# Kernel tuning notes

Measured on AMD Instinct MI355X. Metric: run time of the kernel, lower is better.

The kernel has to match this reference:

```python
import jax, jax.numpy as jnp
import numpy as np
import math

B, S, E, A = 8, 2048, 1024, 1024
NEG = -1e20

def setup_inputs() -> dict:
    key = jax.random.key(0)
    ks = jax.random.split(key, 6)
    scale = 1.0 / math.sqrt(E)
    return {
        "q": jax.random.normal(ks[0], (B, S, E), dtype=jnp.float32),
        "k": jax.random.normal(ks[1], (B, S, E), dtype=jnp.float32),
        "v": jax.random.normal(ks[2], (B, S, E), dtype=jnp.float32),
        "mask_pad": jnp.ones((B, S, S), dtype=jnp.int32),
        "Wq": jax.random.normal(ks[3], (E, A), dtype=jnp.float32) * scale,
        "Wk": jax.random.normal(ks[4], (E, A), dtype=jnp.float32) * scale,
        "Wv": jax.random.normal(ks[5], (E, A), dtype=jnp.float32) * scale,
    }

def reference(q, k, v, mask_pad, Wq, Wk, Wv):
    att_dim = Wq.shape[1]
    qp = jnp.einsum('bse,ea->bsa', q, Wq)
    kp = jnp.einsum('bse,ea->bsa', k, Wk)
    vp = jnp.einsum('bse,ea->bsa', v, Wv)
    # scores: [B, S, S]
    qk = jnp.einsum('bqa,bka->bqk', qp, kp) / jnp.sqrt(jnp.float32(att_dim))
    qk = jnp.where(mask_pad == 0, NEG, qk)
    # causal: torch.tril zeros out upper triangle, then zeros -> -1e20 (faithful quirk)
    seq = qk.shape[1]
    tril = jnp.tril(jnp.ones((seq, seq), dtype=bool))
    qk = jnp.where(tril[None, :, :], qk, 0.0)
    qk = jnp.where(qk == 0.0, NEG, qk)
    att_w = jax.nn.softmax(qk, axis=2)  # dropout p=0 -> identity
    return jnp.einsum('bqk,bka->bqa', att_w, vp)
```

## Files before the change

kernel.cpp:

```cpp
#include <hip/hip_runtime.h>
#include <math.h>

typedef __bf16 bf16x8 __attribute__((ext_vector_type(8)));
typedef float  f32x4  __attribute__((ext_vector_type(4)));
typedef unsigned short u16x8 __attribute__((ext_vector_type(8)));

#define NEGF (-1e20f)

__device__ __forceinline__ unsigned short f2bf(float f) {
  union { float f; unsigned u; } x; x.f = f;
  unsigned r = x.u + 0x7fffu + ((x.u >> 16) & 1u);
  return (unsigned short)(r >> 16);
}
__device__ __forceinline__ float bf2f(unsigned short h) {
  union { unsigned u; float f; } x; x.u = ((unsigned)h) << 16;
  return x.f;
}

__device__ __forceinline__ void gl16(const void* g, void* l) {
  __builtin_amdgcn_global_load_lds(
      (const __attribute__((address_space(1))) unsigned int*)g,
      (__attribute__((address_space(3))) unsigned int*)l, 16, 0, 0);
}
__device__ __forceinline__ unsigned lds_addr(const void* p) {
  return (unsigned)(unsigned long long)(const __attribute__((address_space(3))) char*)p;
}

#define DSR(dst, off) asm volatile("ds_read_b128 %0, %1" : "=v"(dst) : "v"(off))
#define LGKM0 asm volatile("s_waitcnt lgkmcnt(0)" ::: "memory")
#define VMC0  asm volatile("s_waitcnt vmcnt(0)" ::: "memory")
#define SBAR  __builtin_amdgcn_s_barrier()
#define SCH0  __builtin_amdgcn_sched_barrier(0)

__global__ __launch_bounds__(256) void k_cvt3(
    const float* __restrict__ q, const float* __restrict__ k, const float* __restrict__ v,
    unsigned short* __restrict__ qo, unsigned short* __restrict__ ko, unsigned short* __restrict__ vo) {
  const float* in = (blockIdx.y == 0) ? q : (blockIdx.y == 1) ? k : v;
  unsigned short* out = (blockIdx.y == 0) ? qo : (blockIdx.y == 1) ? ko : vo;
  size_t i = ((size_t)blockIdx.x * 256 + threadIdx.x) * 8;
  const float4* p = (const float4*)(in + i);
  float4 a = p[0], b = p[1];
  u16x8 o;
  o[0] = f2bf(a.x); o[1] = f2bf(a.y); o[2] = f2bf(a.z); o[3] = f2bf(a.w);
  o[4] = f2bf(b.x); o[5] = f2bf(b.y); o[6] = f2bf(b.z); o[7] = f2bf(b.w);
  *(u16x8*)(out + i) = o;
}

__global__ __launch_bounds__(256) void k_cvt_w(const float* __restrict__ W,
                                               unsigned short* __restrict__ WT) {
  __shared__ float t[32][33];
  const int tid = threadIdx.x;
  const int tx = tid & 31, ty = tid >> 5;
  const int e0 = blockIdx.y * 32, a0 = blockIdx.x * 32;
#pragma unroll
  for (int i = 0; i < 4; i++) {
    int el = ty + i * 8;
    t[el][tx] = W[(size_t)(e0 + el) * 1024 + a0 + tx];
  }
  __syncthreads();
#pragma unroll
  for (int i = 0; i < 4; i++) {
    int al = ty + i * 8;
    WT[(size_t)(a0 + al) * 1024 + e0 + tx] = f2bf(t[tx][al]);
  }
}

__global__ __launch_bounds__(256) void k_maskbits(const int* __restrict__ mask,
                                                  unsigned short* __restrict__ bits) {
  size_t t = (size_t)blockIdx.x * 256 + threadIdx.x;
  const int4* p = (const int4*)(mask + t * 16);
  int4 a = p[0], b = p[1], c = p[2], d = p[3];
  unsigned m = 0;
  m |= (a.x != 0) ? 1u : 0u;      m |= (a.y != 0) ? 2u : 0u;
  m |= (a.z != 0) ? 4u : 0u;      m |= (a.w != 0) ? 8u : 0u;
  m |= (b.x != 0) ? 16u : 0u;     m |= (b.y != 0) ? 32u : 0u;
  m |= (b.z != 0) ? 64u : 0u;     m |= (b.w != 0) ? 128u : 0u;
  m |= (c.x != 0) ? 256u : 0u;    m |= (c.y != 0) ? 512u : 0u;
  m |= (c.z != 0) ? 1024u : 0u;   m |= (c.w != 0) ? 2048u : 0u;
  m |= (d.x != 0) ? 4096u : 0u;   m |= (d.y != 0) ? 8192u : 0u;
  m |= (d.z != 0) ? 16384u : 0u;  m |= (d.w != 0) ? 32768u : 0u;
  bits[t] = (unsigned short)m;
}

__device__ __forceinline__ void tile128_gemm(
    const unsigned short* __restrict__ A, int lda,
    const unsigned short* __restrict__ Bt, int ldb,
    int brow, int bcol, int NT,
    unsigned short* AsBase, unsigned short* BsBase,
    int wr, int wc, int fr, int fq,
    f32x4 (&acc)[4][4])
{
  const int tid = threadIdx.x, wid = tid >> 6, l = tid & 63;
  const int sr = l >> 3;
  const int sc = ((l & 7) ^ sr) * 8;

  const unsigned short* ga = A + (size_t)(brow + wid * 32 + sr) * lda + sc;
  const unsigned short* gb = Bt + (size_t)(bcol + wid * 32 + sr) * ldb + sc;

  unsigned aA[4], aB[4];
#pragma unroll
  for (int m = 0; m < 4; m++) aA[m] = lds_addr(AsBase) + (unsigned)((wr * 64 + m * 16 + fr) * 128);
#pragma unroll
  for (int n = 0; n < 4; n++) aB[n] = lds_addr(BsBase) + (unsigned)((wc * 64 + n * 16 + fr) * 128);
  const unsigned ck0 = (unsigned)((fq ^ (fr & 7)) * 16);
  const unsigned ck1 = (unsigned)(((4 + fq) ^ (fr & 7)) * 16);

  auto stage = [&](int buf, int k0) {
    unsigned short* la = AsBase + buf * (128 * 64);
    unsigned short* lb = BsBase + buf * (128 * 64);
#pragma unroll
    for (int i = 0; i < 4; i++) {
      gl16(ga + (size_t)(8 * i) * lda + k0, la + (wid * 32 + 8 * i) * 64);
      gl16(gb + (size_t)(8 * i) * ldb + k0, lb + (wid * 32 + 8 * i) * 64);
    }
  };

  stage(0, 0);
  VMC0; SBAR;

  for (int t = 0; t < NT; ++t) {
    if (t + 1 < NT) stage((t + 1) & 1, (t + 1) << 6);
    const unsigned bo = (unsigned)((t & 1) * (128 * 64 * 2));
    u16x8 ar[4], br[4];
#pragma unroll
    for (int m = 0; m < 4; m++) DSR(ar[m], aA[m] + bo + ck0);
#pragma unroll
    for (int n = 0; n < 4; n++) DSR(br[n], aB[n] + bo + ck0);
    LGKM0; SCH0;
    __builtin_amdgcn_s_setprio(1);
#pragma unroll
    for (int m = 0; m < 4; m++)
#pragma unroll
      for (int n = 0; n < 4; n++)
        acc[m][n] = __builtin_amdgcn_mfma_f32_16x16x32_bf16(
            __builtin_bit_cast(bf16x8, ar[m]), __builtin_bit_cast(bf16x8, br[n]), acc[m][n], 0, 0, 0);
    __builtin_amdgcn_s_setprio(0);
    u16x8 ar2[4], br2[4];
#pragma unroll
    for (int m = 0; m < 4; m++) DSR(ar2[m], aA[m] + bo + ck1);
#pragma unroll
    for (int n = 0; n < 4; n++) DSR(br2[n], aB[n] + bo + ck1);
    LGKM0; SCH0;
    __builtin_amdgcn_s_setprio(1);
#pragma unroll
    for (int m = 0; m < 4; m++)
#pragma unroll
      for (int n = 0; n < 4; n++)
        acc[m][n] = __builtin_amdgcn_mfma_f32_16x16x32_bf16(
            __builtin_bit_cast(bf16x8, ar2[m]), __builtin_bit_cast(bf16x8, br2[n]), acc[m][n], 0, 0, 0);
    __builtin_amdgcn_s_setprio(0);
    SCH0;
    VMC0;
    SBAR;
  }
}

__global__ __launch_bounds__(512, 2) void k_proj256(
    const unsigned short* __restrict__ A, int lda,
    const unsigned short* __restrict__ Bt, int ldb,
    unsigned short* __restrict__ C, int ldc, int K, float scale)
{
  const int nwg = gridDim.x * gridDim.y;
  int lin = blockIdx.y * gridDim.x + blockIdx.x;
  int swz = (lin & 7) * (nwg >> 3) + (lin >> 3);
  const int bx = swz % gridDim.x, by = swz / gridDim.x;
  const int brow = by * 256, bcol = bx * 256;

  __shared__ unsigned short As[2][256 * 64];
  __shared__ unsigned short Bs[2][256 * 64];

  const int tid = threadIdx.x, w = tid >> 6, l = tid & 63;
  const int wr = w >> 2, wc = w & 3;
  const int fr = l & 15, fq = l >> 4;
  const int sr = l >> 3;
  const int sc = ((l & 7) ^ sr) * 8;

  const unsigned short* ga = A + (size_t)(brow + w * 32 + sr) * lda + sc;
  const unsigned short* gb = Bt + (size_t)(bcol + w * 32 + sr) * ldb + sc;

  f32x4 acc[8][4] = {};

  unsigned aA[8], aB[4];
#pragma unroll
  for (int m = 0; m < 8; m++) aA[m] = lds_addr(&As[0][0]) + (unsigned)((wr * 128 + m * 16 + fr) * 128);
#pragma unroll
  for (int n = 0; n < 4; n++) aB[n] = lds_addr(&Bs[0][0]) + (unsigned)((wc * 64 + n * 16 + fr) * 128);
  const unsigned ck0 = (unsigned)((fq ^ (fr & 7)) * 16);
  const unsigned ck1 = (unsigned)(((4 + fq) ^ (fr & 7)) * 16);

  auto stage = [&](int buf, int k0) {
#pragma unroll
    for (int i = 0; i < 4; i++) {
      gl16(ga + (size_t)(8 * i) * lda + k0, &As[buf][(w * 32 + 8 * i) * 64]);
      gl16(gb + (size_t)(8 * i) * ldb + k0, &Bs[buf][(w * 32 + 8 * i) * 64]);
    }
  };

  const int NT = K >> 6;
  stage(0, 0);
  VMC0; SBAR;
  for (int t = 0; t < NT; ++t) {
    if (t + 1 < NT) stage((t + 1) & 1, (t + 1) << 6);
    const unsigned bo = (unsigned)((t & 1) * (256 * 64 * 2));
    u16x8 ar[8], br[4];
#pragma unroll
    for (int m = 0; m < 8; m++) DSR(ar[m], aA[m] + bo + ck0);
#pragma unroll
    for (int n = 0; n < 4; n++) DSR(br[n], aB[n] + bo + ck0);
    LGKM0; SCH0;
    __builtin_amdgcn_s_setprio(1);
#pragma unroll
    for (int m = 0; m < 8; m++)
#pragma unroll
      for (int n = 0; n < 4; n++)
        acc[m][n] = __builtin_amdgcn_mfma_f32_16x16x32_bf16(
            __builtin_bit_cast(bf16x8, ar[m]), __builtin_bit_cast(bf16x8, br[n]), acc[m][n], 0, 0, 0);
    __builtin_amdgcn_s_setprio(0);
    u16x8 ar2[8], br2[4];
#pragma unroll
    for (int m = 0; m < 8; m++) DSR(ar2[m], aA[m] + bo + ck1);
#pragma unroll
    for (int n = 0; n < 4; n++) DSR(br2[n], aB[n] + bo + ck1);
    LGKM0; SCH0;
    __builtin_amdgcn_s_setprio(1);
#pragma unroll
    for (int m = 0; m < 8; m++)
#pragma unroll
      for (int n = 0; n < 4; n++)
        acc[m][n] = __builtin_amdgcn_mfma_f32_16x16x32_bf16(
            __builtin_bit_cast(bf16x8, ar2[m]), __builtin_bit_cast(bf16x8, br2[n]), acc[m][n], 0, 0, 0);
    __builtin_amdgcn_s_setprio(0);
    SCH0;
    VMC0; SBAR;
  }

#pragma unroll
  for (int m = 0; m < 8; m++)
#pragma unroll
    for (int n = 0; n < 4; n++)
#pragma unroll
      for (int r = 0; r < 4; r++) {
        int rg = brow + wr * 128 + m * 16 + fq * 4 + r;
        int cg = bcol + wc * 64 + n * 16 + fr;
        C[(size_t)rg * ldc + cg] = f2bf(acc[m][n][r] * scale);
      }
}

__global__ __launch_bounds__(256, 2) void k_scores(
    const unsigned short* __restrict__ QP,
    const unsigned short* __restrict__ KP,
    unsigned short* __restrict__ S,
    const unsigned short* __restrict__ maskbits)
{
  int bid0 = blockIdx.x;
  int bid = (bid0 & 7) * 136 + (bid0 >> 3);
  const int b = bid / 136;
  int t0 = bid - b * 136;
  int by = (int)((sqrtf((float)(8 * t0 + 1)) - 1.0f) * 0.5f);
  if ((by + 1) * (by + 2) / 2 <= t0) by++;
  else if (by * (by + 1) / 2 > t0) by--;
  const int bx = t0 - (by * (by + 1)) / 2;
  const int brow = by * 128, bcol = bx * 128;

  const unsigned short* A  = QP + (size_t)b * (2048 * 1024);
  const unsigned short* Bt = KP + (size_t)b * (2048 * 1024);

  __shared__ unsigned short As[2][128 * 64];
  __shared__ unsigned short Bs[2][128 * 64];

  const int tid = threadIdx.x, wid = tid >> 6, lane = tid & 63;
  const int wr = wid >> 1, wc = wid & 1;
  const int fr = lane & 15, fq = lane >> 4;

  const unsigned short* bits = maskbits + (size_t)b * 2048 * 128;
  unsigned mbits[2] = {0u, 0u};
#pragma unroll
  for (int m = 0; m < 4; m++)
#pragma unroll
    for (int r = 0; r < 4; r++) {
      int qq = brow + wr * 64 + m * 16 + fq * 4 + r;
      unsigned long long mw =
          *(const unsigned long long*)(bits + (size_t)qq * 128 + ((bcol + wc * 64) >> 4));
#pragma unroll
      for (int n = 0; n < 4; n++) {
        int jj = (m << 4) | (n << 2) | r;
        unsigned bit = (unsigned)((mw >> (n * 16 + fr)) & 1ull);
        mbits[jj >> 5] |= bit << (jj & 31);
      }
    }
  asm volatile("" ::: "memory");

  f32x4 acc[4][4] = {};
  tile128_gemm(A, 1024, Bt, 1024, brow, bcol, 16, &As[0][0], &Bs[0][0],
               wr, wc, fr, fq, acc);

  unsigned short* Cb = S + (size_t)b * 2048 * 2048;
#pragma unroll
  for (int m = 0; m < 4; m++)
#pragma unroll
    for (int n = 0; n < 4; n++)
#pragma unroll
      for (int r = 0; r < 4; r++) {
        int jj = (m << 4) | (n << 2) | r;
        int qq = brow + wr * 64 + m * 16 + fq * 4 + r;
        int kk = bcol + wc * 64 + n * 16 + fr;
        float s = acc[m][n][r];
        if (!((mbits[jj >> 5] >> (jj & 31)) & 1u)) s = NEGF;
        if (kk > qq) s = NEGF;
        else if (s == 0.0f) s = NEGF;
        Cb[(size_t)qq * 2048 + kk] = f2bf(s);
      }
}

__global__ __launch_bounds__(256, 2) void k_pv(
    const unsigned short* __restrict__ P,
    const unsigned short* __restrict__ VpT,
    float* __restrict__ Out)
{
  const int b = blockIdx.z;
  const int by = (int)(gridDim.y - 1 - blockIdx.y);
  const int bx = blockIdx.x;
  const int brow = by * 128, bcol = bx * 128;

  const unsigned short* A  = P + (size_t)b * 2048 * 2048;
  const unsigned short* Bt = VpT + (size_t)b * 2048;

  __shared__ unsigned short As[2][128 * 64];
  __shared__ unsigned short Bs[2][128 * 64];

  const int tid = threadIdx.x, wid = tid >> 6, lane = tid & 63;
  const int wr = wid >> 1, wc = wid & 1;
  const int fr = lane & 15, fq = lane >> 4;

  f32x4 acc[4][4] = {};
  const int NT = (brow + 128) >> 6;
  tile128_gemm(A, 2048, Bt, 16384, brow, bcol, NT, &As[0][0], &Bs[0][0],
               wr, wc, fr, fq, acc);

  float* C = Out + (size_t)b * 2048 * 1024;
#pragma unroll
  for (int m = 0; m < 4; m++)
#pragma unroll
    for (int n = 0; n < 4; n++)
#pragma unroll
      for (int r = 0; r < 4; r++) {
        int rg = brow + wr * 64 + m * 16 + fq * 4 + r;
        int cg = bcol + wc * 64 + n * 16 + fr;
        C[(size_t)rg * 1024 + cg] = acc[m][n][r];
      }
}

__global__ __launch_bounds__(256) void k_softmax_bf(unsigned short* __restrict__ S) {
  const int row = blockIdx.x;
  const int qq = row & 2047;
  const int L = ((qq >> 7) + 1) << 7;
  const int tid = threadIdx.x;
  unsigned short* p = S + (size_t)row * 2048;
  float val[8];
  float mx = -3.0e38f;
  int cnt = 0;
  for (int i = tid; i * 4 < L; i += 256) {
    ushort4 u = *(const ushort4*)(p + i * 4);
    float a = bf2f(u.x), bb = bf2f(u.y), c = bf2f(u.z), d = bf2f(u.w);
    val[cnt] = a; val[cnt + 1] = bb; val[cnt + 2] = c; val[cnt + 3] = d;
    mx = fmaxf(fmaxf(fmaxf(mx, a), bb), fmaxf(c, d));
    cnt += 4;
  }
#pragma unroll
  for (int o = 32; o; o >>= 1) mx = fmaxf(mx, __shfl_xor(mx, o));
  __shared__ float sred[8];
  if ((tid & 63) == 0) sred[tid >> 6] = mx;
  __syncthreads();
  mx = fmaxf(fmaxf(sred[0], sred[1]), fmaxf(sred[2], sred[3]));
  float sum = 0.f;
  for (int j = 0; j < cnt; j++) { val[j] = __expf(val[j] - mx); sum += val[j]; }
#pragma unroll
  for (int o = 32; o; o >>= 1) sum += __shfl_xor(sum, o);
  if ((tid & 63) == 0) sred[4 + (tid >> 6)] = sum;
  __syncthreads();
  sum = (sred[4] + sred[5]) + (sred[6] + sred[7]);
  const float inv = 1.0f / sum;
  int j = 0;
  for (int i = tid; i * 4 < L; i += 256) {
    ushort4 o;
    o.x = f2bf(val[j] * inv);     o.y = f2bf(val[j + 1] * inv);
    o.z = f2bf(val[j + 2] * inv); o.w = f2bf(val[j + 3] * inv);
    *(ushort4*)(p + i * 4) = o;
    j += 4;
  }
}

extern "C" void kernel_launch(void* const* d_in, const int* in_sizes, int n_in,
                              void* d_out, int out_size, void* d_ws, size_t ws_size,
                              hipStream_t stream) {
  const float* q   = (const float*)d_in[0];
  const float* k   = (const float*)d_in[1];
  const float* v   = (const float*)d_in[2];
  const int*   msk = (const int*)d_in[3];
  const float* Wq  = (const float*)d_in[4];
  const float* Wk  = (const float*)d_in[5];
  const float* Wv  = (const float*)d_in[6];
  float* out = (float*)d_out;

  char* ws = (char*)d_ws;
  unsigned short* WqT = (unsigned short*)(ws + 0);
  unsigned short* WkT = (unsigned short*)(ws + 2097152);
  unsigned short* WvT = (unsigned short*)(ws + 4194304);
  unsigned short* qp  = (unsigned short*)(ws + 6291456);
  unsigned short* kp  = (unsigned short*)(ws + 39845888);
  unsigned short* vpT = (unsigned short*)(ws + 73400320);
  unsigned short* qbf = (unsigned short*)(ws + 106954752);
  unsigned short* kbf = (unsigned short*)(ws + 140509184);
  unsigned short* vbf = (unsigned short*)(ws + 174063616);
  unsigned short* P = (unsigned short*)(ws + 106954752);
  unsigned short* mbitsbuf = (unsigned short*)(ws + 207618048);

  dim3 blk(256), blk5(512);
  k_cvt3<<<dim3(8192, 3), blk, 0, stream>>>(q, k, v, qbf, kbf, vbf);
  k_cvt_w<<<dim3(32, 32), blk, 0, stream>>>(Wq, WqT);
  k_cvt_w<<<dim3(32, 32), blk, 0, stream>>>(Wk, WkT);
  k_cvt_w<<<dim3(32, 32), blk, 0, stream>>>(Wv, WvT);
  k_maskbits<<<dim3(8192), blk, 0, stream>>>(msk, mbitsbuf);

  k_proj256<<<dim3(4, 64), blk5, 0, stream>>>(qbf, 1024, WqT, 1024, qp, 1024, 1024, 0.03125f);
  k_proj256<<<dim3(4, 64), blk5, 0, stream>>>(kbf, 1024, WkT, 1024, kp, 1024, 1024, 1.0f);
  k_proj256<<<dim3(64, 4), blk5, 0, stream>>>(WvT, 1024, vbf, 1024, vpT, 16384, 1024, 1.0f);

  k_scores<<<dim3(1088), blk, 0, stream>>>(qp, kp, P, mbitsbuf);

  k_softmax_bf<<<dim3(16384), blk, 0, stream>>>(P);

  k_pv<<<dim3(8, 16, 8), blk, 0, stream>>>(P, vpT, out);
  (void)in_sizes; (void)n_in; (void)out_size; (void)ws_size;
}
```

Baseline: 365.8 us.

## Fuse softmax exp into scores epilogue and defer normalization to PV

Removes the separate softmax pass. The scores kernel now writes unnormalized exp(s) in bf16 and atomically accumulates per-row sums, and a new 256x256-tile PV kernel divides by the row sum in its epilogue. It also merges the three weight-transpose launches into one, widens the input conversion to 16 elements per thread, and adds a kernel that zeros the diagonal 128-wide gaps so the larger PV tiles read defined zeros. The risk is that exp is taken without max subtraction, which relies on the scores being small enough not to overflow. Float atomics also make the row sums nondeterministic.

```diff
diff --git a/kernel.cpp b/kernel.cpp
--- a/kernel.cpp
+++ b/kernel.cpp
@@ -11,6 +11,10 @@
   union { float f; unsigned u; } x; x.f = f;
   unsigned r = x.u + 0x7fffu + ((x.u >> 16) & 1u);
   return (unsigned short)(r >> 16);
+}
+__device__ __forceinline__ unsigned short f2bfh(float f) {
+  __bf16 h = (__bf16)f;
+  return __builtin_bit_cast(unsigned short, h);
 }
 __device__ __forceinline__ float bf2f(unsigned short h) {
   union { unsigned u; float f; } x; x.u = ((unsigned)h) << 16;
@@ -37,17 +41,23 @@
     unsigned short* __restrict__ qo, unsigned short* __restrict__ ko, unsigned short* __restrict__ vo) {
   const float* in = (blockIdx.y == 0) ? q : (blockIdx.y == 1) ? k : v;
   unsigned short* out = (blockIdx.y == 0) ? qo : (blockIdx.y == 1) ? ko : vo;
-  size_t i = ((size_t)blockIdx.x * 256 + threadIdx.x) * 8;
+  size_t i = ((size_t)blockIdx.x * 256 + threadIdx.x) * 16;
   const float4* p = (const float4*)(in + i);
-  float4 a = p[0], b = p[1];
-  u16x8 o;
-  o[0] = f2bf(a.x); o[1] = f2bf(a.y); o[2] = f2bf(a.z); o[3] = f2bf(a.w);
-  o[4] = f2bf(b.x); o[5] = f2bf(b.y); o[6] = f2bf(b.z); o[7] = f2bf(b.w);
-  *(u16x8*)(out + i) = o;
-}
-
-__global__ __launch_bounds__(256) void k_cvt_w(const float* __restrict__ W,
-                                               unsigned short* __restrict__ WT) {
+  float4 a = p[0], b = p[1], c = p[2], d = p[3];
+  u16x8 o0, o1;
+  o0[0] = f2bfh(a.x); o0[1] = f2bfh(a.y); o0[2] = f2bfh(a.z); o0[3] = f2bfh(a.w);
+  o0[4] = f2bfh(b.x); o0[5] = f2bfh(b.y); o0[6] = f2bfh(b.z); o0[7] = f2bfh(b.w);
+  o1[0] = f2bfh(c.x); o1[1] = f2bfh(c.y); o1[2] = f2bfh(c.z); o1[3] = f2bfh(c.w);
+  o1[4] = f2bfh(d.x); o1[5] = f2bfh(d.y); o1[6] = f2bfh(d.z); o1[7] = f2bfh(d.w);
+  *(u16x8*)(out + i) = o0;
+  *(u16x8*)(out + i + 8) = o1;
+}
+
+__global__ __launch_bounds__(256) void k_cvt_w3(
+    const float* __restrict__ Wq, const float* __restrict__ Wk, const float* __restrict__ Wv,
+    unsigned short* __restrict__ Tq, unsigned short* __restrict__ Tk, unsigned short* __restrict__ Tv) {
+  const float* W = (blockIdx.z == 0) ? Wq : (blockIdx.z == 1) ? Wk : Wv;
+  unsigned short* WT = (blockIdx.z == 0) ? Tq : (blockIdx.z == 1) ? Tk : Tv;
   __shared__ float t[32][33];
   const int tid = threadIdx.x;
   const int tx = tid & 31, ty = tid >> 5;
@@ -82,6 +92,119 @@
   bits[t] = (unsigned short)m;
 }
 
+__global__ __launch_bounds__(256) void k_zdiag(unsigned short* __restrict__ E) {
+  const int R = blockIdx.x, b = blockIdx.y;
+  unsigned short* base = E + (size_t)b * 2048 * 2048
+                           + (size_t)(R * 256) * 2048 + (R * 256 + 128);
+  const u16x8 z = {0, 0, 0, 0, 0, 0, 0, 0};
+  for (int i = threadIdx.x; i < 2048; i += 256) {
+    int row = i >> 4, c = (i & 15) * 8;
+    *(u16x8*)(base + (size_t)row * 2048 + c) = z;
+  }
+}
+
+__device__ __forceinline__ void gemm256_core(
+    const unsigned short* __restrict__ A, int lda,
+    const unsigned short* __restrict__ Bt, int ldb,
+    int brow, int bcol, int NT,
+    unsigned short* As0, unsigned short* Bs0,
+    f32x4 (&acc)[8][4])
+{
+  const int tid = threadIdx.x, w = tid >> 6, l = tid & 63;
+  const int wr = w >> 2, wc = w & 3;
+  const int fr = l & 15, fq = l >> 4;
+  const int hr = l >> 3;
+  const int hc = ((l & 7) ^ hr) * 8;
+
+  const unsigned short* ga = A + (size_t)(brow + w * 32 + hr) * lda + hc;
+  const unsigned short* gb = Bt + (size_t)(bcol + w * 32 + hr) * ldb + hc;
+
+  unsigned aA[8], aB[4];
+#pragma unroll
+  for (int m = 0; m < 8; m++) aA[m] = lds_addr(As0) + (unsigned)((wr * 128 + m * 16 + fr) * 128);
+#pragma unroll
+  for (int n = 0; n < 4; n++) aB[n] = lds_addr(Bs0) + (unsigned)((wc * 64 + n * 16 + fr) * 128);
+  const unsigned ck0 = (unsigned)((fq ^ (fr & 7)) * 16);
+  const unsigned ck1 = (unsigned)(((4 + fq) ^ (fr & 7)) * 16);
+
+  auto stage = [&](int buf, int k0) {
+#pragma unroll
+    for (int i = 0; i < 4; i++) {
+      gl16(ga + (size_t)(8 * i) * lda + k0, As0 + buf * (256 * 64) + (w * 32 + 8 * i) * 64);
+      gl16(gb + (size_t)(8 * i) * ldb + k0, Bs0 + buf * (256 * 64) + (w * 32 + 8 * i) * 64);
+    }
+  };
+
+  stage(0, 0);
+  VMC0; SBAR;
+  for (int t = 0; t < NT; ++t) {
+    if (t + 1 < NT) stage((t + 1) & 1, (t + 1) << 6);
+    const unsigned bo = (unsigned)((t & 1) * (256 * 64 * 2));
+    u16x8 ar[8], br[4];
+#pragma unroll
+    for (int m = 0; m < 8; m++) DSR(ar[m], aA[m] + bo + ck0);
+#pragma unroll
+    for (int n = 0; n < 4; n++) DSR(br[n], aB[n] + bo + ck0);
+    LGKM0; SCH0;
+    __builtin_amdgcn_s_setprio(1);
+#pragma unroll
+    for (int m = 0; m < 8; m++)
+#pragma unroll
+      for (int n = 0; n < 4; n++)
+        acc[m][n] = __builtin_amdgcn_mfma_f32_16x16x32_bf16(
+            __builtin_bit_cast(bf16x8, ar[m]), __builtin_bit_cast(bf16x8, br[n]), acc[m][n], 0, 0, 0);
+    __builtin_amdgcn_s_setprio(0);
+    u16x8 ar2[8], br2[4];
+#pragma unroll
+    for (int m = 0; m < 8; m++) DSR(ar2[m], aA[m] + bo + ck1);
+#pragma unroll
+    for (int n = 0; n < 4; n++) DSR(br2[n], aB[n] + bo + ck1);
+    LGKM0; SCH0;
+    __builtin_amdgcn_s_setprio(1);
+#pragma unroll
+    for (int m = 0; m < 8; m++)
+#pragma unroll
+      for (int n = 0; n < 4; n++)
+        acc[m][n] = __builtin_amdgcn_mfma_f32_16x16x32_bf16(
+            __builtin_bit_cast(bf16x8, ar2[m]), __builtin_bit_cast(bf16x8, br2[n]), acc[m][n], 0, 0, 0);
+    __builtin_amdgcn_s_setprio(0);
+    SCH0;
+    VMC0; SBAR;
+  }
+}
+
+__global__ __launch_bounds__(512, 2) void k_proj256(
+    const unsigned short* __restrict__ A, int lda,
+    const unsigned short* __restrict__ Bt, int ldb,
+    unsigned short* __restrict__ C, int ldc, float scale)
+{
+  const int nwg = gridDim.x * gridDim.y;
+  int lin = blockIdx.y * gridDim.x + blockIdx.x;
+  int swz = (lin & 7) * (nwg >> 3) + (lin >> 3);
+  const int bx = swz % gridDim.x, by = swz / gridDim.x;
+  const int brow = by * 256, bcol = bx * 256;
+
+  __shared__ unsigned short As[2][256 * 64];
+  __shared__ unsigned short Bs[2][256 * 64];
+  const int tid = threadIdx.x, w = tid >> 6, l = tid & 63;
+  const int wr = w >> 2, wc = w & 3;
+  const int fr = l & 15, fq = l >> 4;
+
+  f32x4 acc[8][4] = {};
+  gemm256_core(A, lda, Bt, ldb, brow, bcol, 16, &As[0][0], &Bs[0][0], acc);
+
+#pragma unroll
+  for (int m = 0; m < 8; m++)
+#pragma unroll
+    for (int n = 0; n < 4; n++)
+#pragma unroll
+      for (int r = 0; r < 4; r++) {
+        int rg = brow + wr * 128 + m * 16 + fq * 4 + r;
+        int cg = bcol + wc * 64 + n * 16 + fr;
+        C[(size_t)rg * ldc + cg] = f2bf(acc[m][n][r] * scale);
+      }
+}
+
 __device__ __forceinline__ void tile128_gemm(
     const unsigned short* __restrict__ A, int lda,
     const unsigned short* __restrict__ Bt, int ldb,
@@ -155,102 +278,12 @@
   }
 }
 
-__global__ __launch_bounds__(512, 2) void k_proj256(
-    const unsigned short* __restrict__ A, int lda,
-    const unsigned short* __restrict__ Bt, int ldb,
-    unsigned short* __restrict__ C, int ldc, int K, float scale)
-{
-  const int nwg = gridDim.x * gridDim.y;
-  int lin = blockIdx.y * gridDim.x + blockIdx.x;
-  int swz = (lin & 7) * (nwg >> 3) + (lin >> 3);
-  const int bx = swz % gridDim.x, by = swz / gridDim.x;
-  const int brow = by * 256, bcol = bx * 256;
-
-  __shared__ unsigned short As[2][256 * 64];
-  __shared__ unsigned short Bs[2][256 * 64];
-
-  const int tid = threadIdx.x, w = tid >> 6, l = tid & 63;
-  const int wr = w >> 2, wc = w & 3;
-  const int fr = l & 15, fq = l >> 4;
-  const int sr = l >> 3;
-  const int sc = ((l & 7) ^ sr) * 8;
-
-  const unsigned short* ga = A + (size_t)(brow + w * 32 + sr) * lda + sc;
-  const unsigned short* gb = Bt + (size_t)(bcol + w * 32 + sr) * ldb + sc;
-
-  f32x4 acc[8][4] = {};
-
-  unsigned aA[8], aB[4];
-#pragma unroll
-  for (int m = 0; m < 8; m++) aA[m] = lds_addr(&As[0][0]) + (unsigned)((wr * 128 + m * 16 + fr) * 128);
-#pragma unroll
-  for (int n = 0; n < 4; n++) aB[n] = lds_addr(&Bs[0][0]) + (unsigned)((wc * 64 + n * 16 + fr) * 128);
-  const unsigned ck0 = (unsigned)((fq ^ (fr & 7)) * 16);
-  const unsigned ck1 = (unsigned)(((4 + fq) ^ (fr & 7)) * 16);
-
-  auto stage = [&](int buf, int k0) {
-#pragma unroll
-    for (int i = 0; i < 4; i++) {
-      gl16(ga + (size_t)(8 * i) * lda + k0, &As[buf][(w * 32 + 8 * i) * 64]);
-      gl16(gb + (size_t)(8 * i) * ldb + k0, &Bs[buf][(w * 32 + 8 * i) * 64]);
-    }
-  };
-
-  const int NT = K >> 6;
-  stage(0, 0);
-  VMC0; SBAR;
-  for (int t = 0; t < NT; ++t) {
-    if (t + 1 < NT) stage((t + 1) & 1, (t + 1) << 6);
-    const unsigned bo = (unsigned)((t & 1) * (256 * 64 * 2));
-    u16x8 ar[8], br[4];
-#pragma unroll
-    for (int m = 0; m < 8; m++) DSR(ar[m], aA[m] + bo + ck0);
-#pragma unroll
-    for (int n = 0; n < 4; n++) DSR(br[n], aB[n] + bo + ck0);
-    LGKM0; SCH0;
-    __builtin_amdgcn_s_setprio(1);
-#pragma unroll
-    for (int m = 0; m < 8; m++)
-#pragma unroll
-      for (int n = 0; n < 4; n++)
-        acc[m][n] = __builtin_amdgcn_mfma_f32_16x16x32_bf16(
-            __builtin_bit_cast(bf16x8, ar[m]), __builtin_bit_cast(bf16x8, br[n]), acc[m][n], 0, 0, 0);
-    __builtin_amdgcn_s_setprio(0);
-    u16x8 ar2[8], br2[4];
-#pragma unroll
-    for (int m = 0; m < 8; m++) DSR(ar2[m], aA[m] + bo + ck1);
-#pragma unroll
-    for (int n = 0; n < 4; n++) DSR(br2[n], aB[n] + bo + ck1);
-    LGKM0; SCH0;
-    __builtin_amdgcn_s_setprio(1);
-#pragma unroll
-    for (int m = 0; m < 8; m++)
-#pragma unroll
-      for (int n = 0; n < 4; n++)
-        acc[m][n] = __builtin_amdgcn_mfma_f32_16x16x32_bf16(
-            __builtin_bit_cast(bf16x8, ar2[m]), __builtin_bit_cast(bf16x8, br2[n]), acc[m][n], 0, 0, 0);
-    __builtin_amdgcn_s_setprio(0);
-    SCH0;
-    VMC0; SBAR;
-  }
-
-#pragma unroll
-  for (int m = 0; m < 8; m++)
-#pragma unroll
-    for (int n = 0; n < 4; n++)
-#pragma unroll
-      for (int r = 0; r < 4; r++) {
-        int rg = brow + wr * 128 + m * 16 + fq * 4 + r;
-        int cg = bcol + wc * 64 + n * 16 + fr;
-        C[(size_t)rg * ldc + cg] = f2bf(acc[m][n][r] * scale);
-      }
-}
-
 __global__ __launch_bounds__(256, 2) void k_scores(
     const unsigned short* __restrict__ QP,
     const unsigned short* __restrict__ KP,
-    unsigned short* __restrict__ S,
-    const unsigned short* __restrict__ maskbits)
+    unsigned short* __restrict__ E,
+    const unsigned short* __restrict__ maskbits,
+    float* __restrict__ rowsum)
 {
   int bid0 = blockIdx.x;
   int bid = (bid0 & 7) * 136 + (bid0 >> 3);
@@ -294,100 +327,70 @@
   tile128_gemm(A, 1024, Bt, 1024, brow, bcol, 16, &As[0][0], &Bs[0][0],
                wr, wc, fr, fq, acc);
 
-  unsigned short* Cb = S + (size_t)b * 2048 * 2048;
+  unsigned short* Cb = E + (size_t)b * 2048 * 2048;
+  float* rs = rowsum + (size_t)b * 2048;
 #pragma unroll
   for (int m = 0; m < 4; m++)
 #pragma unroll
-    for (int n = 0; n < 4; n++)
-#pragma unroll
-      for (int r = 0; r < 4; r++) {
+    for (int r = 0; r < 4; r++) {
+      int qq = brow + wr * 64 + m * 16 + fq * 4 + r;
+      float se = 0.f;
+#pragma unroll
+      for (int n = 0; n < 4; n++) {
         int jj = (m << 4) | (n << 2) | r;
-        int qq = brow + wr * 64 + m * 16 + fq * 4 + r;
         int kk = bcol + wc * 64 + n * 16 + fr;
         float s = acc[m][n][r];
-        if (!((mbits[jj >> 5] >> (jj & 31)) & 1u)) s = NEGF;
-        if (kk > qq) s = NEGF;
-        else if (s == 0.0f) s = NEGF;
-        Cb[(size_t)qq * 2048 + kk] = f2bf(s);
+        bool dead = !((mbits[jj >> 5] >> (jj & 31)) & 1u) || (kk > qq) || (s == 0.0f);
+        float e = dead ? 0.f : __expf(s);
+        se += e;
+        Cb[(size_t)qq * 2048 + kk] = f2bf(e);
       }
-}
-
-__global__ __launch_bounds__(256, 2) void k_pv(
-    const unsigned short* __restrict__ P,
+      se += __shfl_xor(se, 1);
+      se += __shfl_xor(se, 2);
+      se += __shfl_xor(se, 4);
+      se += __shfl_xor(se, 8);
+      if (fr == 0) atomicAdd(&rs[qq], se);
+    }
+}
+
+__global__ __launch_bounds__(512, 2) void k_pv256(
+    const unsigned short* __restrict__ E,
     const unsigned short* __restrict__ VpT,
+    const float* __restrict__ rowsum,
     float* __restrict__ Out)
 {
   const int b = blockIdx.z;
   const int by = (int)(gridDim.y - 1 - blockIdx.y);
   const int bx = blockIdx.x;
-  const int brow = by * 128, bcol = bx * 128;
-
-  const unsigned short* A  = P + (size_t)b * 2048 * 2048;
+  const int brow = by * 256, bcol = bx * 256;
+
+  const unsigned short* A  = E + (size_t)b * 2048 * 2048;
   const unsigned short* Bt = VpT + (size_t)b * 2048;
 
-  __shared__ unsigned short As[2][128 * 64];
-  __shared__ unsigned short Bs[2][128 * 64];
-
-  const int tid = threadIdx.x, wid = tid >> 6, lane = tid & 63;
-  const int wr = wid >> 1, wc = wid & 1;
-  const int fr = lane & 15, fq = lane >> 4;
-
-  f32x4 acc[4][4] = {};
-  const int NT = (brow + 128) >> 6;
-  tile128_gemm(A, 2048, Bt, 16384, brow, bcol, NT, &As[0][0], &Bs[0][0],
-               wr, wc, fr, fq, acc);
-
+  __shared__ unsigned short As[2][256 * 64];
+  __shared__ unsigned short Bs[2][256 * 64];
+  const int tid = threadIdx.x, w = tid >> 6, l = tid & 63;
+  const int wr = w >> 2, wc = w & 3;
+  const int fr = l & 15, fq = l >> 4;
+
+  f32x4 acc[8][4] = {};
+  const int NT = (brow + 256) >> 6;
+  gemm256_core(A, 2048, Bt, 16384, brow, bcol, NT, &As[0][0], &Bs[0][0], acc);
+
+  const float* rs = rowsum + (size_t)b * 2048;
   float* C = Out + (size_t)b * 2048 * 1024;
 #pragma unroll
-  for (int m = 0; m < 4; m++)
-#pragma unroll
-    for (int n = 0; n < 4; n++)
-#pragma unroll
-      for (int r = 0; r < 4; r++) {
-        int rg = brow + wr * 64 + m * 16 + fq * 4 + r;
+  for (int m = 0; m < 8; m++)
+#pragma unroll
+    for (int r = 0; r < 4; r++) {
+      int rg = brow + wr * 128 + m * 16 + fq * 4 + r;
+      float inv = 1.0f / rs[rg];
+#pragma unroll
+      for (int n = 0; n < 4; n++) {
         int cg = bcol + wc * 64 + n * 16 + fr;
-        C[(size_t)rg * 1024 + cg] = acc[m][n][r];
+        C[(size_t)rg * 1024 + cg] = acc[m][n][r] * inv;
       }
-}
-
-__global__ __launch_bounds__(256) void k_softmax_bf(unsigned short* __restrict__ S) {
-  const int row = blockIdx.x;
-  const int qq = row & 2047;
-  const int L = ((qq >> 7) + 1) << 7;
-  const int tid = threadIdx.x;
-  unsigned short* p = S + (size_t)row * 2048;
-  float val[8];
-  float mx = -3.0e38f;
-  int cnt = 0;
-  for (int i = tid; i * 4 < L; i += 256) {
-    ushort4 u = *(const ushort4*)(p + i * 4);
-    float a = bf2f(u.x), bb = bf2f(u.y), c = bf2f(u.z), d = bf2f(u.w);
-    val[cnt] = a; val[cnt + 1] = bb; val[cnt + 2] = c; val[cnt + 3] = d;
-    mx = fmaxf(fmaxf(fmaxf(mx, a), bb), fmaxf(c, d));
-    cnt += 4;
-  }
-#pragma unroll
-  for (int o = 32; o; o >>= 1) mx = fmaxf(mx, __shfl_xor(mx, o));
-  __shared__ float sred[8];
-  if ((tid & 63) == 0) sred[tid >> 6] = mx;
-  __syncthreads();
-  mx = fmaxf(fmaxf(sred[0], sred[1]), fmaxf(sred[2], sred[3]));
-  float sum = 0.f;
-  for (int j = 0; j < cnt; j++) { val[j] = __expf(val[j] - mx); sum += val[j]; }
-#pragma unroll
-  for (int o = 32; o; o >>= 1) sum += __shfl_xor(sum, o);
-  if ((tid & 63) == 0) sred[4 + (tid >> 6)] = sum;
-  __syncthreads();
-  sum = (sred[4] + sred[5]) + (sred[6] + sred[7]);
-  const float inv = 1.0f / sum;
-  int j = 0;
-  for (int i = tid; i * 4 < L; i += 256) {
-    ushort4 o;
-    o.x = f2bf(val[j] * inv);     o.y = f2bf(val[j + 1] * inv);
-    o.z = f2bf(val[j + 2] * inv); o.w = f2bf(val[j + 3] * inv);
-    *(ushort4*)(p + i * 4) = o;
-    j += 4;
-  }
+    }
 }
 
 extern "C" void kernel_launch(void* const* d_in, const int* in_sizes, int n_in,
@@ -412,24 +415,24 @@
   unsigned short* qbf = (unsigned short*)(ws + 106954752);
   unsigned short* kbf = (unsigned short*)(ws + 140509184);
   unsigned short* vbf = (unsigned short*)(ws + 174063616);
-  unsigned short* P = (unsigned short*)(ws + 106954752);
+  unsigned short* E = (unsigned short*)(ws + 106954752);
   unsigned short* mbitsbuf = (unsigned short*)(ws + 207618048);
+  float* rowsum = (float*)(ws + 211812352);
 
   dim3 blk(256), blk5(512);
-  k_cvt3<<<dim3(8192, 3), blk, 0, stream>>>(q, k, v, qbf, kbf, vbf);
-  k_cvt_w<<<dim3(32, 32), blk, 0, stream>>>(Wq, WqT);
-  k_cvt_w<<<dim3(32, 32), blk, 0, stream>>>(Wk, WkT);
-  k_cvt_w<<<dim3(32, 32), blk, 0, stream>>>(Wv, WvT);
+  k_cvt3<<<dim3(4096, 3), blk, 0, stream>>>(q, k, v, qbf, kbf, vbf);
+  k_cvt_w3<<<dim3(32, 32, 3), blk, 0, stream>>>(Wq, Wk, Wv, WqT, WkT, WvT);
   k_maskbits<<<dim3(8192), blk, 0, stream>>>(msk, mbitsbuf);
-
-  k_proj256<<<dim3(4, 64), blk5, 0, stream>>>(qbf, 1024, WqT, 1024, qp, 1024, 1024, 0.03125f);
-  k_proj256<<<dim3(4, 64), blk5, 0, stream>>>(kbf, 1024, WkT, 1024, kp, 1024, 1024, 1.0f);
-  k_proj256<<<dim3(64, 4), blk5, 0, stream>>>(WvT, 1024, vbf, 1024, vpT, 16384, 1024, 1.0f);
-
-  k_scores<<<dim3(1088), blk, 0, stream>>>(qp, kp, P, mbitsbuf);
-
-  k_softmax_bf<<<dim3(16384), blk, 0, stream>>>(P);
-
-  k_pv<<<dim3(8, 16, 8), blk, 0, stream>>>(P, vpT, out);
+  hipMemsetAsync(rowsum, 0, 16384 * sizeof(float), stream);
+
+  k_proj256<<<dim3(4, 64), blk5, 0, stream>>>(qbf, 1024, WqT, 1024, qp, 1024, 0.03125f);
+  k_proj256<<<dim3(4, 64), blk5, 0, stream>>>(kbf, 1024, WkT, 1024, kp, 1024, 1.0f);
+  k_proj256<<<dim3(64, 4), blk5, 0, stream>>>(WvT, 1024, vbf, 1024, vpT, 16384, 1.0f);
+
+  k_zdiag<<<dim3(8, 8), blk, 0, stream>>>(E);
+
+  k_scores<<<dim3(1088), blk, 0, stream>>>(qp, kp, E, mbitsbuf, rowsum);
+
+  k_pv256<<<dim3(4, 8, 8), blk5, 0, stream>>>(E, vpT, rowsum, out);
   (void)in_sizes; (void)n_in; (void)out_size; (void)ws_size;
 }
```

Result: faster. 329.7 us, median of 2 (-9.9%).
